# Kernel optimization log

Measured on AMD Instinct MI355X. Metric: run time of the kernel, lower is better.

Reference implementation:

```python
import jax, jax.numpy as jnp
from jax import lax
import numpy as np
import math

B = 8
SEQ_LEN = 2048
LABEL_LEN = 1024
PRED_LEN = 1024
DEC_LEN = LABEL_LEN + PRED_LEN
ENC_IN = 7; DEC_IN = 7; C_OUT = 7
D_MODEL = 512; N_HEADS = 8; D_FF = 512
E_LAYERS = 3; D_LAYERS = 2
MOVING_AVG = 25; FACTOR = 5


def _fixed_table(n, d):
    # sinusoidal FixedEmbedding table (non-learned)
    pos = np.arange(n, dtype=np.float32)[:, None]
    div = np.exp(np.arange(0, d, 2, dtype=np.float32) * (-math.log(10000.0) / d))
    w = np.zeros((n, d), np.float32)
    w[:, 0::2] = np.sin(pos * div)
    w[:, 1::2] = np.cos(pos * div)
    return jnp.asarray(w)

MONTH_T = _fixed_table(13, D_MODEL)
DAY_T = _fixed_table(32, D_MODEL)
WEEKDAY_T = _fixed_table(7, D_MODEL)
HOUR_T = _fixed_table(24, D_MODEL)


def temporal_embed(x_mark):  # [B,L,4] int -> [B,L,D]
    return (MONTH_T[x_mark[..., 0]] + DAY_T[x_mark[..., 1]]
            + WEEKDAY_T[x_mark[..., 2]] + HOUR_T[x_mark[..., 3]])


def circ_conv3(x, W):  # Conv1d(k=3, pad=1, circular, no bias); x [B,L,Cin], W [3,Cin,Cout]
    xp = jnp.concatenate([x[:, -1:], x, x[:, :1]], axis=1)
    return xp[:, :-2] @ W[0] + xp[:, 1:-1] @ W[1] + xp[:, 2:] @ W[2]


def series_decomp(x, k=MOVING_AVG):  # moving-average decomposition
    pad = (k - 1) // 2
    xp = jnp.concatenate([jnp.repeat(x[:, :1], pad, axis=1), x,
                          jnp.repeat(x[:, -1:], pad, axis=1)], axis=1)
    mov = lax.reduce_window(xp, 0.0, lax.add, (1, k, 1), (1, 1, 1), 'VALID') / k
    return x - mov, mov


def my_layernorm(x, w, b):  # LayerNorm then subtract seasonal (time-mean) bias
    mu = jnp.mean(x, axis=-1, keepdims=True)
    var = jnp.var(x, axis=-1, keepdims=True)
    xh = (x - mu) * lax.rsqrt(var + 1e-5) * w + b
    return xh - jnp.mean(xh, axis=1, keepdims=True)


def gelu(x):
    return jax.nn.gelu(x, approximate=False)


def autocorrelation(q, k, v):  # q [B,L,H,E], k/v [B,S,H,E]
    Bq, L, H, E = q.shape
    S = k.shape[1]
    if L > S:
        k = jnp.pad(k, ((0, 0), (0, L - S), (0, 0), (0, 0)))
        v = jnp.pad(v, ((0, 0), (0, L - S), (0, 0), (0, 0)))
    else:
        k = k[:, :L]; v = v[:, :L]
    qf = jnp.fft.rfft(q.transpose(0, 2, 3, 1), axis=-1)  # [B,H,E,Lf]
    kf = jnp.fft.rfft(k.transpose(0, 2, 3, 1), axis=-1)
    corr = jnp.fft.irfft(qf * jnp.conj(kf), n=L, axis=-1)  # [B,H,E,L]
    vv = v.transpose(0, 2, 3, 1)  # [B,H,E,L]
    top_k = int(FACTOR * math.log(L))
    mean_value = jnp.mean(corr, axis=(1, 2))  # [B,L]
    index = lax.top_k(jnp.mean(mean_value, axis=0), top_k)[1]  # [top_k], shared over batch (training path)
    tmp_corr = jax.nn.softmax(mean_value[:, index], axis=-1)  # [B,top_k]
    base = jnp.arange(L)
    def step(acc, iw):
        idx, w = iw
        pattern = jnp.take(vv, (base + idx) % L, axis=-1)  # roll by -idx
        return acc + pattern * w[:, None, None, None], None
    agg, _ = lax.scan(step, jnp.zeros_like(vv), (index, tmp_corr.T))
    return agg.transpose(0, 3, 1, 2)  # [B,L,H,E]


def attn_layer(qx, kx, vx, Wq, bq, Wk, bk, Wv, bv, Wo, bo):
    Bq, L, _ = qx.shape
    S = kx.shape[1]
    q = (qx @ Wq + bq).reshape(Bq, L, N_HEADS, -1)
    k = (kx @ Wk + bk).reshape(Bq, S, N_HEADS, -1)
    v = (vx @ Wv + bv).reshape(Bq, S, N_HEADS, -1)
    out = autocorrelation(q, k, v).reshape(Bq, L, -1)
    return out @ Wo + bo


def _forward(x_enc, x_dec, emb_enc_W, emb_dec_W,
             enc_Wq, enc_bq, enc_Wk, enc_bk, enc_Wv, enc_bv, enc_Wo, enc_bo,
             enc_c1, enc_c2, enc_norm_w, enc_norm_b,
             dec_sWq, dec_sbq, dec_sWk, dec_sbk, dec_sWv, dec_sbv, dec_sWo, dec_sbo,
             dec_cWq, dec_cbq, dec_cWk, dec_cbk, dec_cWv, dec_cbv, dec_cWo, dec_cbo,
             dec_c1, dec_c2, dec_trendW, dec_norm_w, dec_norm_b, proj_W, proj_b,
             x_mark_enc, x_mark_dec):
    Bq = x_enc.shape[0]
    mean = jnp.broadcast_to(jnp.mean(x_enc, axis=1, keepdims=True), (Bq, PRED_LEN, x_enc.shape[2]))
    seasonal_init, trend_init = series_decomp(x_enc)
    trend_init = jnp.concatenate([trend_init[:, -LABEL_LEN:], mean], axis=1)
    zeros = jnp.zeros((Bq, PRED_LEN, x_dec.shape[2]), x_enc.dtype)
    seasonal_init = jnp.concatenate([seasonal_init[:, -LABEL_LEN:], zeros], axis=1)

    # encoder
    enc_out = circ_conv3(x_enc, emb_enc_W) + temporal_embed(x_mark_enc)
    for l in range(E_LAYERS):
        new_x = attn_layer(enc_out, enc_out, enc_out,
                           enc_Wq[l], enc_bq[l], enc_Wk[l], enc_bk[l],
                           enc_Wv[l], enc_bv[l], enc_Wo[l], enc_bo[l])
        x, _ = series_decomp(enc_out + new_x)
        y = gelu(x @ enc_c1[l]) @ enc_c2[l]
        enc_out, _ = series_decomp(x + y)
    enc_out = my_layernorm(enc_out, enc_norm_w, enc_norm_b)

    # decoder
    dec_out = circ_conv3(seasonal_init, emb_dec_W) + temporal_embed(x_mark_dec)
    trend = trend_init
    for l in range(D_LAYERS):
        x = dec_out + attn_layer(dec_out, dec_out, dec_out,
                                 dec_sWq[l], dec_sbq[l], dec_sWk[l], dec_sbk[l],
                                 dec_sWv[l], dec_sbv[l], dec_sWo[l], dec_sbo[l])
        x, t1 = series_decomp(x)
        x = x + attn_layer(x, enc_out, enc_out,
                           dec_cWq[l], dec_cbq[l], dec_cWk[l], dec_cbk[l],
                           dec_cWv[l], dec_cbv[l], dec_cWo[l], dec_cbo[l])
        x, t2 = series_decomp(x)
        y = gelu(x @ dec_c1[l]) @ dec_c2[l]
        dec_out, t3 = series_decomp(x + y)
        trend = trend + circ_conv3(t1 + t2 + t3, dec_trendW[l])  # d_model -> c_out
    dec_out = my_layernorm(dec_out, dec_norm_w, dec_norm_b)
    seasonal_part = dec_out @ proj_W + proj_b
    out = trend + seasonal_part
    return out[:, -PRED_LEN:, :]


def setup_inputs() -> dict:
    key = jax.random.key(0)
    keys = jax.random.split(key, 60)
    ki = iter(range(60))
    def rn(*s):
        return jax.random.normal(keys[next(ki)], s, dtype=jnp.float32) * 0.02
    inp = {}
    inp['x_enc'] = jax.random.normal(keys[next(ki)], (B, SEQ_LEN, ENC_IN), dtype=jnp.float32)
    inp['x_mark_enc'] = jax.random.randint(keys[next(ki)], (B, SEQ_LEN, 4), 0, 7)
    inp['x_dec'] = jax.random.normal(keys[next(ki)], (B, DEC_LEN, DEC_IN), dtype=jnp.float32)
    inp['x_mark_dec'] = jax.random.randint(keys[next(ki)], (B, DEC_LEN, 4), 0, 7)
    inp['emb_enc_W'] = rn(3, ENC_IN, D_MODEL)
    inp['emb_dec_W'] = rn(3, DEC_IN, D_MODEL)
    for n in ('Wq', 'Wk', 'Wv', 'Wo'):
        bn = 'b' + n[1]
        inp['enc_' + n] = rn(E_LAYERS, D_MODEL, D_MODEL)
        inp['enc_' + bn] = rn(E_LAYERS, D_MODEL)
        inp['dec_s' + n] = rn(D_LAYERS, D_MODEL, D_MODEL)
        inp['dec_s' + bn] = rn(D_LAYERS, D_MODEL)
        inp['dec_c' + n] = rn(D_LAYERS, D_MODEL, D_MODEL)
        inp['dec_c' + bn] = rn(D_LAYERS, D_MODEL)
    inp['enc_c1'] = rn(E_LAYERS, D_MODEL, D_FF)
    inp['enc_c2'] = rn(E_LAYERS, D_FF, D_MODEL)
    inp['enc_norm_w'] = jnp.ones((D_MODEL,), jnp.float32)
    inp['enc_norm_b'] = jnp.zeros((D_MODEL,), jnp.float32)
    inp['dec_c1'] = rn(D_LAYERS, D_MODEL, D_FF)
    inp['dec_c2'] = rn(D_LAYERS, D_FF, D_MODEL)
    inp['dec_trendW'] = rn(D_LAYERS, 3, D_MODEL, C_OUT)
    inp['dec_norm_w'] = jnp.ones((D_MODEL,), jnp.float32)
    inp['dec_norm_b'] = jnp.zeros((D_MODEL,), jnp.float32)
    inp['proj_W'] = rn(D_MODEL, C_OUT)
    inp['proj_b'] = jnp.zeros((C_OUT,), jnp.float32)
    return inp


def reference(x_enc, x_mark_enc, x_dec, x_mark_dec, emb_enc_W, emb_dec_W,
              enc_Wq, enc_bq, enc_Wk, enc_bk, enc_Wv, enc_bv, enc_Wo, enc_bo,
              enc_c1, enc_c2, enc_norm_w, enc_norm_b,
              dec_sWq, dec_sbq, dec_sWk, dec_sbk, dec_sWv, dec_sbv, dec_sWo, dec_sbo,
              dec_cWq, dec_cbq, dec_cWk, dec_cbk, dec_cWv, dec_cbv, dec_cWo, dec_cbo,
              dec_c1, dec_c2, dec_trendW, dec_norm_w, dec_norm_b, proj_W, proj_b):
    return _forward(x_enc, x_dec, emb_enc_W, emb_dec_W,
                    enc_Wq, enc_bq, enc_Wk, enc_bk, enc_Wv, enc_bv, enc_Wo, enc_bo,
                    enc_c1, enc_c2, enc_norm_w, enc_norm_b,
                    dec_sWq, dec_sbq, dec_sWk, dec_sbk, dec_sWv, dec_sbv, dec_sWo, dec_sbo,
                    dec_cWq, dec_cbq, dec_cWk, dec_cbk, dec_cWv, dec_cbv, dec_cWo, dec_cbo,
                    dec_c1, dec_c2, dec_trendW, dec_norm_w, dec_norm_b, proj_W, proj_b,
                    x_mark_enc, x_mark_dec)
```

## Files before the change

kernel.cpp:

```cpp
#include <hip/hip_runtime.h>
#include <math.h>

#define BATCH 8
#define LSEQ 2048
#define DMODEL 512
#define TOPK 38
#define MROWS (BATCH * LSEQ)

typedef __attribute__((ext_vector_type(8))) short bf16x8;
typedef __attribute__((ext_vector_type(4))) float f32x4;

__device__ __forceinline__ float wave_sum(float v) {
#pragma unroll
  for (int off = 32; off > 0; off >>= 1) v += __shfl_down(v, off);
  return v;
}

__device__ __forceinline__ short f2bf(float f) {
  unsigned u = __float_as_uint(f);
  unsigned r = (u + 0x7fffu + ((u >> 16) & 1u)) >> 16;
  return (short)r;
}

__global__ void table_init_kernel(float* __restrict__ tab, float2* __restrict__ twg) {
  int i = blockIdx.x * 256 + threadIdx.x;
  if (i < 7 * DMODEL) {
    int p = i >> 9;
    int d = i & (DMODEL - 1);
    float div = expf((float)(d >> 1) * (-2.0f * 9.210340371976184f / 512.0f));
    float ang = (float)p * div;
    tab[i] = (d & 1) ? cosf(ang) : sinf(ang);
  }
  if (i < 1024) {
    float ang = -6.283185307179586f * (float)i / 2048.0f;
    float sn, cs;
    sincosf(ang, &sn, &cs);
    twg[i] = make_float2(cs, sn);
  }
}

__global__ __launch_bounds__(256) void embed_kernel(
    const float* __restrict__ x,
    const float* __restrict__ W,
    const int* __restrict__ mark,
    const float* __restrict__ tab,
    float* __restrict__ out)
{
  __shared__ float xs[21];
  int bt = blockIdx.x;
  int b = bt >> 11, t = bt & (LSEQ - 1);
  int tid = threadIdx.x;
  if (tid < 21) {
    int j = tid / 7, c = tid - j * 7;
    int row = (t - 1 + j + LSEQ) & (LSEQ - 1);
    xs[tid] = x[((size_t)b * LSEQ + row) * 7 + c];
  }
  __syncthreads();
  const int* mk = mark + ((size_t)b * LSEQ + t) * 4;
  int m0 = mk[0], m1 = mk[1], m2 = mk[2], m3 = mk[3];
#pragma unroll
  for (int h = 0; h < 2; ++h) {
    int d = tid + h * 256;
    float acc = tab[m0 * DMODEL + d] + tab[m1 * DMODEL + d] +
                tab[m2 * DMODEL + d] + tab[m3 * DMODEL + d];
#pragma unroll
    for (int j = 0; j < 3; ++j)
#pragma unroll
      for (int c = 0; c < 7; ++c)
        acc += xs[j * 7 + c] * W[(size_t)((j * 7 + c) * DMODEL) + d];
    out[((size_t)b * LSEQ + t) * DMODEL + d] = acc;
  }
}

__global__ void decomp_kernel(const float* __restrict__ x, float* __restrict__ seas,
                              float* __restrict__ trend, int D, int mode)
{
  int bt = blockIdx.x;
  int b = bt >> 11, t = bt & (LSEQ - 1);
  const float* xb = x + (size_t)b * LSEQ * D;
  for (int d = threadIdx.x; d < D; d += blockDim.x) {
    float s = 0.f;
#pragma unroll
    for (int o = -12; o <= 12; ++o) {
      int tt = t + o;
      tt = tt < 0 ? 0 : (tt > LSEQ - 1 ? LSEQ - 1 : tt);
      s += xb[(size_t)tt * D + d];
    }
    float mov = s / 25.0f;
    size_t idx = ((size_t)b * LSEQ + t) * D + d;
    seas[idx] = x[idx] - mov;
    if (mode == 1) trend[idx] = mov;
    else if (mode == 2) trend[idx] += mov;
  }
}

__global__ __launch_bounds__(256) void sgemm_kernel(
    const float* __restrict__ A, const float* __restrict__ B,
    const float* __restrict__ bias, float* __restrict__ C,
    int M, int N, int K)
{
  __shared__ float As[16][132];
  __shared__ float Bs[16][132];
  int m0 = blockIdx.x * 128;
  int n0 = blockIdx.y * 128;
  int tid = threadIdx.x;
  int tx = tid & 15, ty = tid >> 4;
  float acc[8][8];
#pragma unroll
  for (int i = 0; i < 8; ++i)
#pragma unroll
    for (int j = 0; j < 8; ++j) acc[i][j] = 0.f;

  int ar = tid >> 2;
  int ac = (tid & 3) << 2;
  int br = tid >> 5;
  int bc = (tid & 31) << 2;

  for (int k0 = 0; k0 < K; k0 += 16) {
    float4 a0 = *(const float4*)(A + (size_t)(m0 + ar) * K + k0 + ac);
    float4 a1 = *(const float4*)(A + (size_t)(m0 + 64 + ar) * K + k0 + ac);
    float4 b0 = *(const float4*)(B + (size_t)(k0 + br) * N + n0 + bc);
    float4 b1 = *(const float4*)(B + (size_t)(k0 + 8 + br) * N + n0 + bc);
    As[ac + 0][ar] = a0.x; As[ac + 1][ar] = a0.y; As[ac + 2][ar] = a0.z; As[ac + 3][ar] = a0.w;
    As[ac + 0][64 + ar] = a1.x; As[ac + 1][64 + ar] = a1.y; As[ac + 2][64 + ar] = a1.z; As[ac + 3][64 + ar] = a1.w;
    *(float4*)&Bs[br][bc] = b0;
    *(float4*)&Bs[br + 8][bc] = b1;
    __syncthreads();
#pragma unroll
    for (int k = 0; k < 16; ++k) {
      float av[8], bv[8];
      *(float4*)(av)     = *(const float4*)&As[k][ty * 8];
      *(float4*)(av + 4) = *(const float4*)&As[k][ty * 8 + 4];
      *(float4*)(bv)     = *(const float4*)&Bs[k][tx * 8];
      *(float4*)(bv + 4) = *(const float4*)&Bs[k][tx * 8 + 4];
#pragma unroll
      for (int i = 0; i < 8; ++i)
#pragma unroll
        for (int j = 0; j < 8; ++j)
          acc[i][j] = fmaf(av[i], bv[j], acc[i][j]);
    }
    __syncthreads();
  }
#pragma unroll
  for (int i = 0; i < 8; ++i) {
    int m = m0 + ty * 8 + i;
    float* cr = C + (size_t)m * N + n0 + tx * 8;
#pragma unroll
    for (int j = 0; j < 8; j += 4) {
      float4 v = make_float4(acc[i][j], acc[i][j + 1], acc[i][j + 2], acc[i][j + 3]);
      if (bias) {
        const float* bp = bias + n0 + tx * 8 + j;
        v.x += bp[0]; v.y += bp[1]; v.z += bp[2]; v.w += bp[3];
      }
      *(float4*)(cr + j) = v;
    }
  }
}

__global__ void prep_wt_kernel(const float* __restrict__ W, short* __restrict__ Wt) {
  __shared__ float tile[32][33];
  int k0 = blockIdx.x << 5, n0 = blockIdx.y << 5;
  for (int i = threadIdx.y; i < 32; i += 8)
    tile[i][threadIdx.x] = W[(size_t)(k0 + i) * DMODEL + n0 + threadIdx.x];
  __syncthreads();
  for (int i = threadIdx.y; i < 32; i += 8)
    Wt[(size_t)(n0 + i) * DMODEL + k0 + threadIdx.x] = f2bf(tile[threadIdx.x][i]);
}

__global__ __launch_bounds__(256) void gemm_bf16_kernel(
    const float* __restrict__ A, const short* __restrict__ Wt,
    const float* __restrict__ bias, float* __restrict__ C)
{
  const int K = DMODEL, N = DMODEL;
  __shared__ short As[128][40];
  __shared__ short Bs[128][40];
  int m0 = blockIdx.x * 128;
  int n0 = blockIdx.y * 128;
  int tid = threadIdx.x;
  int lane = tid & 63;
  int wave = tid >> 6;
  int wm = (wave >> 1) * 64;
  int wn = (wave & 1) * 64;
  int lr = lane & 15;
  int lk = (lane >> 4) * 8;

  f32x4 acc[4][4];
#pragma unroll
  for (int i = 0; i < 4; ++i)
#pragma unroll
    for (int j = 0; j < 4; ++j) acc[i][j] = (f32x4){0.f, 0.f, 0.f, 0.f};

  for (int k0 = 0; k0 < K; k0 += 32) {
#pragma unroll
    for (int i = 0; i < 4; ++i) {
      int f = tid + i * 256;
      int row = f >> 3, c4 = (f & 7) << 2;
      float4 v = *(const float4*)(A + (size_t)(m0 + row) * K + k0 + c4);
      short4 s = make_short4(f2bf(v.x), f2bf(v.y), f2bf(v.z), f2bf(v.w));
      *(short4*)&As[row][c4] = s;
    }
#pragma unroll
    for (int i = 0; i < 2; ++i) {
      int f = tid + i * 256;
      int row = f >> 2, c8 = (f & 3) << 3;
      *(int4*)&Bs[row][c8] = *(const int4*)(Wt + (size_t)(n0 + row) * K + k0 + c8);
    }
    __syncthreads();
    bf16x8 af[4], bfr[4];
#pragma unroll
    for (int m = 0; m < 4; ++m) af[m] = *(const bf16x8*)&As[wm + m * 16 + lr][lk];
#pragma unroll
    for (int n = 0; n < 4; ++n) bfr[n] = *(const bf16x8*)&Bs[wn + n * 16 + lr][lk];
#pragma unroll
    for (int m = 0; m < 4; ++m)
#pragma unroll
      for (int n = 0; n < 4; ++n)
        acc[m][n] = __builtin_amdgcn_mfma_f32_16x16x32_bf16(af[m], bfr[n], acc[m][n], 0, 0, 0);
    __syncthreads();
  }
  int orow = m0 + wm + (lane >> 4) * 4;
  int ocol = n0 + wn + lr;
#pragma unroll
  for (int m = 0; m < 4; ++m)
#pragma unroll
    for (int n = 0; n < 4; ++n) {
      int col = ocol + n * 16;
      float bv = bias ? bias[col] : 0.f;
#pragma unroll
      for (int r = 0; r < 4; ++r)
        C[(size_t)(orow + m * 16 + r) * N + col] = acc[m][n][r] + bv;
    }
}

__global__ void transpose_kernel(const float* __restrict__ in, float* __restrict__ out) {
  __shared__ float tile[32][33];
  int b = blockIdx.x;
  int r0 = blockIdx.y << 5;
  int c0 = blockIdx.z << 5;
  const float* ib = in + (size_t)b * LSEQ * DMODEL;
  float* ob = out + (size_t)b * LSEQ * DMODEL;
  for (int i = threadIdx.y; i < 32; i += 8)
    tile[i][threadIdx.x] = ib[(size_t)(r0 + i) * DMODEL + c0 + threadIdx.x];
  __syncthreads();
  for (int i = threadIdx.y; i < 32; i += 8)
    ob[(size_t)(c0 + i) * LSEQ + r0 + threadIdx.x] = tile[threadIdx.x][i];
}

__device__ __forceinline__ void fft2048_lds(float2* buf, const float2* tw, int tid, int inverse) {
#pragma unroll 1
  for (int s = 1; s <= 11; ++s) {
    int half = 1 << (s - 1);
#pragma unroll 1
    for (int bf = tid; bf < 1024; bf += 256) {
      int j = bf & (half - 1);
      int i0 = ((bf >> (s - 1)) << s) | j;
      int i1 = i0 + half;
      float2 w = tw[j << (11 - s)];
      float wy = inverse ? -w.y : w.y;
      float2 a = buf[i0], b = buf[i1];
      float tr = b.x * w.x - b.y * wy;
      float ti = b.x * wy + b.y * w.x;
      buf[i0] = make_float2(a.x + tr, a.y + ti);
      buf[i1] = make_float2(a.x - tr, a.y - ti);
    }
    __syncthreads();
  }
}

__global__ __launch_bounds__(256) void corr_spectrum_kernel(
    const float* __restrict__ qt, const float* __restrict__ kt,
    const float2* __restrict__ twg, float2* __restrict__ partial)
{
  __shared__ float2 buf[2048];
  __shared__ float2 acc[2048];
  __shared__ float2 twl[1024];
  int tid = threadIdx.x;
  int b = blockIdx.x >> 6;
  int g = blockIdx.x & 63;
  for (int i = tid; i < 1024; i += 256) twl[i] = twg[i];
  for (int i = tid; i < 2048; i += 256) acc[i] = make_float2(0.f, 0.f);
  __syncthreads();
#pragma unroll 1
  for (int ch = 0; ch < 8; ++ch) {
    int d = (g << 3) + ch;
    const float* qr = qt + ((size_t)b * DMODEL + d) * LSEQ;
    const float* kr = kt + ((size_t)b * DMODEL + d) * LSEQ;
    for (int i = tid; i < 2048; i += 256) {
      int rev = __brev((unsigned)i) >> 21;
      buf[rev] = make_float2(qr[i], kr[i]);
    }
    __syncthreads();
    fft2048_lds(buf, twl, tid, 0);
    for (int i = tid; i < 2048; i += 256) {
      float2 z1 = buf[i];
      float2 z2 = buf[(2048 - i) & 2047];
      float Qr = 0.5f * (z1.x + z2.x);
      float Qi = 0.5f * (z1.y - z2.y);
      float Kr = 0.5f * (z1.y + z2.y);
      float Ki = -0.5f * (z1.x - z2.x);
      acc[i].x += Qr * Kr + Qi * Ki;
      acc[i].y += Qi * Kr - Qr * Ki;
    }
    __syncthreads();
  }
  float2* op = partial + (size_t)blockIdx.x * 2048;
  for (int i = tid; i < 2048; i += 256) op[i] = acc[i];
}

__global__ __launch_bounds__(256) void reduce_partials_kernel(
    const float2* __restrict__ partial, float2* __restrict__ spec)
{
  int b = blockIdx.x;
  int i = blockIdx.y * 256 + threadIdx.x;
  const float2* pp = partial + ((size_t)b * 64) * 2048 + i;
  float sx = 0.f, sy = 0.f;
#pragma unroll 8
  for (int g = 0; g < 64; ++g) {
    float2 v = pp[(size_t)g * 2048];
    sx += v.x; sy += v.y;
  }
  spec[(size_t)b * 2048 + i] = make_float2(sx, sy);
}

__global__ __launch_bounds__(256) void ifft_kernel(
    const float2* __restrict__ spec, const float2* __restrict__ twg,
    float* __restrict__ mv)
{
  __shared__ float2 buf[2048];
  __shared__ float2 twl[1024];
  int tid = threadIdx.x;
  int b = blockIdx.x;
  for (int i = tid; i < 1024; i += 256) twl[i] = twg[i];
  for (int i = tid; i < 2048; i += 256) {
    int rev = __brev((unsigned)i) >> 21;
    buf[rev] = spec[(size_t)b * 2048 + i];
  }
  __syncthreads();
  fft2048_lds(buf, twl, tid, 1);
  const float scale = 1.0f / (2048.0f * 512.0f);
  for (int i = tid; i < 2048; i += 256) mv[(size_t)b * 2048 + i] = buf[i].x * scale;
}

__global__ void topk_kernel(const float* __restrict__ mv, int* __restrict__ idxOut,
                            float* __restrict__ wOut)
{
  __shared__ float cm[2048];
  __shared__ float rmax[256];
  __shared__ int rIdx[256];
  __shared__ int sIdx[TOPK];
  int tid = threadIdx.x;
  for (int i = tid; i < 2048; i += 256) {
    float s = 0.f;
#pragma unroll
    for (int b = 0; b < BATCH; ++b) s += mv[(size_t)b * 2048 + i];
    cm[i] = s;
  }
  __syncthreads();
  for (int it = 0; it < TOPK; ++it) {
    float best = -1e30f; int bi = 0;
    for (int i = tid; i < 2048; i += 256)
      if (cm[i] > best) { best = cm[i]; bi = i; }
    rmax[tid] = best; rIdx[tid] = bi;
    __syncthreads();
    for (int s = 128; s > 0; s >>= 1) {
      if (tid < s && rmax[tid + s] > rmax[tid]) { rmax[tid] = rmax[tid + s]; rIdx[tid] = rIdx[tid + s]; }
      __syncthreads();
    }
    if (tid == 0) { sIdx[it] = rIdx[0]; idxOut[it] = rIdx[0]; cm[rIdx[0]] = -1e30f; }
    __syncthreads();
  }
  if (tid < BATCH) {
    int b = tid;
    float vals[TOPK];
    float m = -1e30f;
    for (int j = 0; j < TOPK; ++j) { vals[j] = mv[(size_t)b * 2048 + sIdx[j]]; m = fmaxf(m, vals[j]); }
    float s = 0.f;
    for (int j = 0; j < TOPK; ++j) { vals[j] = expf(vals[j] - m); s += vals[j]; }
    for (int j = 0; j < TOPK; ++j) wOut[b * TOPK + j] = vals[j] / s;
  }
}

__global__ __launch_bounds__(256) void shift_sum_kernel(
    const float* __restrict__ v, const int* __restrict__ idx,
    const float* __restrict__ w, float* __restrict__ out)
{
  __shared__ int sidx[TOPK];
  __shared__ float sw[TOPK];
  int bt = blockIdx.x;
  int b = bt & 7, t = bt >> 3;
  int tid = threadIdx.x;
  if (tid < TOPK) { sidx[tid] = idx[tid]; sw[tid] = w[b * TOPK + tid]; }
  __syncthreads();
  float a0 = 0.f, a1 = 0.f;
  const float* vb = v + (size_t)b * LSEQ * DMODEL;
#pragma unroll 1
  for (int j = 0; j < TOPK; ++j) {
    int row = (t + sidx[j]) & (LSEQ - 1);
    const float* vr = vb + (size_t)row * DMODEL;
    a0 = fmaf(sw[j], vr[tid], a0);
    a1 = fmaf(sw[j], vr[tid + 256], a1);
  }
  size_t o = ((size_t)b * LSEQ + t) * DMODEL;
  out[o + tid] = a0;
  out[o + tid + 256] = a1;
}

__global__ void add_kernel(const float* __restrict__ a, const float* __restrict__ b,
                           float* __restrict__ c, int n4)
{
  int i = blockIdx.x * blockDim.x + threadIdx.x;
  int stride = gridDim.x * blockDim.x;
  const float4* A = (const float4*)a;
  const float4* B = (const float4*)b;
  float4* C = (float4*)c;
  for (; i < n4; i += stride) {
    float4 x = A[i], y = B[i];
    C[i] = make_float4(x.x + y.x, x.y + y.y, x.z + y.z, x.w + y.w);
  }
}

__global__ void gelu_kernel(float* __restrict__ x, int n4) {
  int i = blockIdx.x * blockDim.x + threadIdx.x;
  int stride = gridDim.x * blockDim.x;
  float4* X = (float4*)x;
  const float k = 0.7071067811865475f;
  for (; i < n4; i += stride) {
    float4 v = X[i];
    v.x = 0.5f * v.x * (1.f + erff(v.x * k));
    v.y = 0.5f * v.y * (1.f + erff(v.y * k));
    v.z = 0.5f * v.z * (1.f + erff(v.z * k));
    v.w = 0.5f * v.w * (1.f + erff(v.w * k));
    X[i] = v;
  }
}

__global__ __launch_bounds__(256) void layernorm_kernel(
    const float* __restrict__ x, const float* __restrict__ w,
    const float* __restrict__ bb, float* __restrict__ out)
{
  __shared__ float red[256];
  int row = blockIdx.x;
  int tid = threadIdx.x;
  const float* xr = x + (size_t)row * DMODEL;
  float v0 = xr[tid], v1 = xr[tid + 256];
  red[tid] = v0 + v1;
  __syncthreads();
  for (int o = 128; o > 0; o >>= 1) {
    if (tid < o) red[tid] += red[tid + o];
    __syncthreads();
  }
  float mu = red[0] / 512.0f;
  __syncthreads();
  float d0 = v0 - mu, d1 = v1 - mu;
  red[tid] = d0 * d0 + d1 * d1;
  __syncthreads();
  for (int o = 128; o > 0; o >>= 1) {
    if (tid < o) red[tid] += red[tid + o];
    __syncthreads();
  }
  float var = red[0] / 512.0f;
  float inv = 1.0f / sqrtf(var + 1e-5f);
  out[(size_t)row * DMODEL + tid] = d0 * inv * w[tid] + bb[tid];
  out[(size_t)row * DMODEL + tid + 256] = d1 * inv * w[tid + 256] + bb[tid + 256];
}

__global__ __launch_bounds__(256) void colsum_kernel(const float* __restrict__ x,
                                                     float* __restrict__ part)
{
  int b = blockIdx.x, ch = blockIdx.y;
  const float* xb = x + ((size_t)b * LSEQ + (size_t)ch * 128) * DMODEL;
  float s0 = 0.f, s1 = 0.f;
#pragma unroll 1
  for (int t = 0; t < 128; ++t) {
    s0 += xb[(size_t)t * DMODEL + threadIdx.x];
    s1 += xb[(size_t)t * DMODEL + threadIdx.x + 256];
  }
  part[(size_t)(b * 16 + ch) * DMODEL + threadIdx.x] = s0;
  part[(size_t)(b * 16 + ch) * DMODEL + threadIdx.x + 256] = s1;
}

__global__ void colmean_finish_kernel(const float* __restrict__ part, float* __restrict__ mu) {
  int i = blockIdx.x * 256 + threadIdx.x;
  if (i < BATCH * DMODEL) {
    int b = i / DMODEL, d = i - b * DMODEL;
    float s = 0.f;
#pragma unroll
    for (int c = 0; c < 16; ++c) s += part[(size_t)(b * 16 + c) * DMODEL + d];
    mu[i] = s / (float)LSEQ;
  }
}

__global__ __launch_bounds__(256) void sub_colmean_kernel(
    const float* __restrict__ x, const float* __restrict__ mu, float* __restrict__ out)
{
  int bt = blockIdx.x;
  int b = bt >> 11;
  size_t base = (size_t)bt * DMODEL;
  int d0 = threadIdx.x, d1 = threadIdx.x + 256;
  out[base + d0] = x[base + d0] - mu[b * DMODEL + d0];
  out[base + d1] = x[base + d1] - mu[b * DMODEL + d1];
}

__global__ void mean_enc_kernel(const float* __restrict__ x, float* __restrict__ mean7) {
  int b = blockIdx.x / 7, c = blockIdx.x % 7;
  float s = 0.f;
  for (int t = threadIdx.x; t < LSEQ; t += 64) s += x[((size_t)b * LSEQ + t) * 7 + c];
  s = wave_sum(s);
  if (threadIdx.x == 0) mean7[b * 7 + c] = s / 2048.0f;
}

__global__ void build_inits_kernel(const float* __restrict__ seas7, const float* __restrict__ trend7,
                                   const float* __restrict__ mean7,
                                   float* __restrict__ seasonal_init, float* __restrict__ trend_acc)
{
  int i = blockIdx.x * 256 + threadIdx.x;
  if (i >= BATCH * LSEQ * 7) return;
  int c = i % 7;
  int bt = i / 7;
  int t = bt & (LSEQ - 1);
  int b = bt >> 11;
  if (t < 1024) {
    size_t src = ((size_t)b * LSEQ + (t + 1024)) * 7 + c;
    seasonal_init[i] = seas7[src];
    trend_acc[i] = trend7[src];
  } else {
    seasonal_init[i] = 0.f;
    trend_acc[i] = mean7[b * 7 + c];
  }
}

__global__ void trend_conv_kernel(const float* __restrict__ x, const float* __restrict__ W,
                                  float* __restrict__ trend)
{
  int bt = blockIdx.x;
  int b = bt >> 11, t = bt & (LSEQ - 1);
  int lane = threadIdx.x;
  float acc[7] = {0, 0, 0, 0, 0, 0, 0};
#pragma unroll
  for (int j = 0; j < 3; ++j) {
    int row = (t - 1 + j + LSEQ) & (LSEQ - 1);
    const float* xr = x + ((size_t)b * LSEQ + row) * DMODEL;
    const float* wj = W + (size_t)j * DMODEL * 7;
    for (int d = lane; d < DMODEL; d += 64) {
      float xv = xr[d];
      const float* wr = wj + d * 7;
#pragma unroll
      for (int c = 0; c < 7; ++c) acc[c] += xv * wr[c];
    }
  }
#pragma unroll
  for (int c = 0; c < 7; ++c) {
    float s = wave_sum(acc[c]);
    if (lane == 0) trend[((size_t)b * LSEQ + t) * 7 + c] += s;
  }
}

__global__ void final_proj_kernel(const float* __restrict__ x, const float* __restrict__ W,
                                  const float* __restrict__ bias, const float* __restrict__ trend,
                                  float* __restrict__ out)
{
  int bt = blockIdx.x;
  int b = bt >> 10, tt = bt & 1023;
  int t = tt + 1024;
  int lane = threadIdx.x;
  const float* xr = x + ((size_t)b * LSEQ + t) * DMODEL;
  float acc[7] = {0, 0, 0, 0, 0, 0, 0};
  for (int d = lane; d < DMODEL; d += 64) {
    float xv = xr[d];
    const float* wr = W + d * 7;
#pragma unroll
    for (int c = 0; c < 7; ++c) acc[c] += xv * wr[c];
  }
#pragma unroll
  for (int c = 0; c < 7; ++c) {
    float s = wave_sum(acc[c]);
    if (lane == 0)
      out[((size_t)b * 1024 + tt) * 7 + c] = s + bias[c] + trend[((size_t)b * LSEQ + t) * 7 + c];
  }
}

static inline void launch_sgemm(const float* A, const float* W, const float* bias, float* C,
                                hipStream_t s)
{
  sgemm_kernel<<<dim3(MROWS / 128, DMODEL / 128), dim3(256), 0, s>>>(
      A, W, bias, C, MROWS, DMODEL, DMODEL);
}

static inline void launch_gemm_bf16(const float* A, const float* W, const float* bias, float* C,
                                    short* wtScratch, hipStream_t s)
{
  prep_wt_kernel<<<dim3(16, 16), dim3(32, 8), 0, s>>>(W, wtScratch);
  gemm_bf16_kernel<<<dim3(MROWS / 128, DMODEL / 128), dim3(256), 0, s>>>(A, wtScratch, bias, C);
}

struct AttnScratch {
  float2* partial;
  float2* spec;
  float* mv;
  int* idx;
  float* w;
  const float2* twg;
  short* wt;
};

static void run_attn(const float* qx, const float* kx, const float* vx,
                     const float* Wq, const float* bq, const float* Wk, const float* bk,
                     const float* Wv, const float* bv, const float* Wo, const float* bo,
                     float* t1, float* t2, float* t3, const AttnScratch& sc, hipStream_t s)
{
  dim3 tg(BATCH, LSEQ / 32, DMODEL / 32);
  launch_sgemm(qx, Wq, bq, t1, s);
  transpose_kernel<<<tg, dim3(32, 8), 0, s>>>(t1, t2);
  launch_sgemm(kx, Wk, bk, t1, s);
  transpose_kernel<<<tg, dim3(32, 8), 0, s>>>(t1, t3);
  launch_gemm_bf16(vx, Wv, bv, t1, sc.wt, s);
  corr_spectrum_kernel<<<dim3(BATCH * 64), dim3(256), 0, s>>>(t2, t3, sc.twg, sc.partial);
  reduce_partials_kernel<<<dim3(BATCH, 8), dim3(256), 0, s>>>(sc.partial, sc.spec);
  ifft_kernel<<<dim3(BATCH), dim3(256), 0, s>>>(sc.spec, sc.twg, sc.mv);
  topk_kernel<<<dim3(1), dim3(256), 0, s>>>(sc.mv, sc.idx, sc.w);
  shift_sum_kernel<<<dim3(MROWS), dim3(256), 0, s>>>(t1, sc.idx, sc.w, t2);
  launch_gemm_bf16(t2, Wo, bo, t3, sc.wt, s);
}

extern "C" void kernel_launch(void* const* d_in, const int* in_sizes, int n_in,
                              void* d_out, int out_size, void* d_ws, size_t ws_size,
                              hipStream_t stream)
{
  if (n_in < 41) return;

  const float* x_enc    = (const float*)d_in[0];
  const int*   mark_enc = (const int*)d_in[1];
  const int*   mark_dec = (const int*)d_in[3];
  const float* emb_enc_W = (const float*)d_in[4];
  const float* emb_dec_W = (const float*)d_in[5];
  const float* enc_Wq = (const float*)d_in[6];
  const float* enc_bq = (const float*)d_in[7];
  const float* dec_sWq = (const float*)d_in[8];
  const float* dec_sbq = (const float*)d_in[9];
  const float* dec_cWq = (const float*)d_in[10];
  const float* dec_cbq = (const float*)d_in[11];
  const float* enc_Wk = (const float*)d_in[12];
  const float* enc_bk = (const float*)d_in[13];
  const float* dec_sWk = (const float*)d_in[14];
  const float* dec_sbk = (const float*)d_in[15];
  const float* dec_cWk = (const float*)d_in[16];
  const float* dec_cbk = (const float*)d_in[17];
  const float* enc_Wv = (const float*)d_in[18];
  const float* enc_bv = (const float*)d_in[19];
  const float* dec_sWv = (const float*)d_in[20];
  const float* dec_sbv = (const float*)d_in[21];
  const float* dec_cWv = (const float*)d_in[22];
  const float* dec_cbv = (const float*)d_in[23];
  const float* enc_Wo = (const float*)d_in[24];
  const float* enc_bo = (const float*)d_in[25];
  const float* dec_sWo = (const float*)d_in[26];
  const float* dec_sbo = (const float*)d_in[27];
  const float* dec_cWo = (const float*)d_in[28];
  const float* dec_cbo = (const float*)d_in[29];
  const float* enc_c1 = (const float*)d_in[30];
  const float* enc_c2 = (const float*)d_in[31];
  const float* enc_nw = (const float*)d_in[32];
  const float* enc_nb = (const float*)d_in[33];
  const float* dec_c1 = (const float*)d_in[34];
  const float* dec_c2 = (const float*)d_in[35];
  const float* dec_trendW = (const float*)d_in[36];
  const float* dec_nw = (const float*)d_in[37];
  const float* dec_nb = (const float*)d_in[38];
  const float* proj_W = (const float*)d_in[39];
  const float* proj_b = (const float*)d_in[40];

  (void)in_sizes; (void)out_size;

  const size_t BIG = (size_t)MROWS * DMODEL * sizeof(float);
  char* p = (char*)d_ws;
  float* enc_out = (float*)p; p += BIG;
  float* dec_out = (float*)p; p += BIG;
  float* tsum    = (float*)p; p += BIG;
  float* b1 = (float*)p; p += BIG;
  float* b2 = (float*)p; p += BIG;
  float* b3 = (float*)p; p += BIG;
  float2* partial = (float2*)p; p += (size_t)BATCH * 64 * 2048 * sizeof(float2);
  float2* specbuf = (float2*)p; p += (size_t)BATCH * 2048 * sizeof(float2);
  short* wtScratch = (short*)p; p += (size_t)DMODEL * DMODEL * sizeof(short);
  float* mv = (float*)p; p += (size_t)BATCH * 2048 * sizeof(float);
  float* tab = (float*)p; p += 7 * DMODEL * sizeof(float);
  float2* twg = (float2*)p; p += 1024 * sizeof(float2);
  float* seas7 = (float*)p; p += (size_t)BATCH * LSEQ * 7 * sizeof(float);
  float* trend7tmp = (float*)p; p += (size_t)BATCH * LSEQ * 7 * sizeof(float);
  float* seasonal_init = (float*)p; p += (size_t)BATCH * LSEQ * 7 * sizeof(float);
  float* trend_acc = (float*)p; p += (size_t)BATCH * LSEQ * 7 * sizeof(float);
  float* colpart = (float*)p; p += (size_t)BATCH * 16 * DMODEL * sizeof(float);
  float* colmu = (float*)p; p += (size_t)BATCH * DMODEL * sizeof(float);
  float* mean7 = (float*)p; p += 256;
  int* idxbuf = (int*)p; p += 256;
  float* wbuf = (float*)p; p += 2048;
  if ((size_t)(p - (char*)d_ws) > ws_size) return;

  const int n4 = MROWS * DMODEL / 4;
  AttnScratch sc{partial, specbuf, mv, idxbuf, wbuf, twg, wtScratch};

  table_init_kernel<<<dim3(14), dim3(256), 0, stream>>>(tab, twg);
  decomp_kernel<<<dim3(MROWS), dim3(64), 0, stream>>>(x_enc, seas7, trend7tmp, 7, 1);
  mean_enc_kernel<<<dim3(56), dim3(64), 0, stream>>>(x_enc, mean7);
  build_inits_kernel<<<dim3((BATCH * LSEQ * 7 + 255) / 256), dim3(256), 0, stream>>>(
      seas7, trend7tmp, mean7, seasonal_init, trend_acc);
  embed_kernel<<<dim3(MROWS), dim3(256), 0, stream>>>(x_enc, emb_enc_W, mark_enc, tab, enc_out);
  embed_kernel<<<dim3(MROWS), dim3(256), 0, stream>>>(seasonal_init, emb_dec_W, mark_dec, tab, dec_out);

  for (int l = 0; l < 3; ++l) {
    size_t wOff = (size_t)l * DMODEL * DMODEL, bOff = (size_t)l * DMODEL;
    run_attn(enc_out, enc_out, enc_out,
             enc_Wq + wOff, enc_bq + bOff, enc_Wk + wOff, enc_bk + bOff,
             enc_Wv + wOff, enc_bv + bOff, enc_Wo + wOff, enc_bo + bOff,
             b1, b2, b3, sc, stream);
    add_kernel<<<dim3(2048), dim3(256), 0, stream>>>(enc_out, b3, b1, n4);
    decomp_kernel<<<dim3(MROWS), dim3(256), 0, stream>>>(b1, b2, nullptr, DMODEL, 0);
    launch_gemm_bf16(b2, enc_c1 + wOff, nullptr, b3, wtScratch, stream);
    gelu_kernel<<<dim3(2048), dim3(256), 0, stream>>>(b3, n4);
    launch_gemm_bf16(b3, enc_c2 + wOff, nullptr, b1, wtScratch, stream);
    add_kernel<<<dim3(2048), dim3(256), 0, stream>>>(b2, b1, b3, n4);
    decomp_kernel<<<dim3(MROWS), dim3(256), 0, stream>>>(b3, enc_out, nullptr, DMODEL, 0);
  }
  layernorm_kernel<<<dim3(MROWS), dim3(256), 0, stream>>>(enc_out, enc_nw, enc_nb, b1);
  colsum_kernel<<<dim3(BATCH, 16), dim3(256), 0, stream>>>(b1, colpart);
  colmean_finish_kernel<<<dim3(16), dim3(256), 0, stream>>>(colpart, colmu);
  sub_colmean_kernel<<<dim3(MROWS), dim3(256), 0, stream>>>(b1, colmu, enc_out);

  for (int l = 0; l < 2; ++l) {
    size_t wOff = (size_t)l * DMODEL * DMODEL, bOff = (size_t)l * DMODEL;
    run_attn(dec_out, dec_out, dec_out,
             dec_sWq + wOff, dec_sbq + bOff, dec_sWk + wOff, dec_sbk + bOff,
             dec_sWv + wOff, dec_sbv + bOff, dec_sWo + wOff, dec_sbo + bOff,
             b1, b2, b3, sc, stream);
    add_kernel<<<dim3(2048), dim3(256), 0, stream>>>(dec_out, b3, b1, n4);
    decomp_kernel<<<dim3(MROWS), dim3(256), 0, stream>>>(b1, b2, tsum, DMODEL, 1);
    run_attn(b2, enc_out, enc_out,
             dec_cWq + wOff, dec_cbq + bOff, dec_cWk + wOff, dec_cbk + bOff,
             dec_cWv + wOff, dec_cbv + bOff, dec_cWo + wOff, dec_cbo + bOff,
             b1, b3, dec_out, sc, stream);
    add_kernel<<<dim3(2048), dim3(256), 0, stream>>>(b2, dec_out, b1, n4);
    decomp_kernel<<<dim3(MROWS), dim3(256), 0, stream>>>(b1, b3, tsum, DMODEL, 2);
    launch_gemm_bf16(b3, dec_c1 + wOff, nullptr, b1, wtScratch, stream);
    gelu_kernel<<<dim3(2048), dim3(256), 0, stream>>>(b1, n4);
    launch_gemm_bf16(b1, dec_c2 + wOff, nullptr, b2, wtScratch, stream);
    add_kernel<<<dim3(2048), dim3(256), 0, stream>>>(b3, b2, b1, n4);
    decomp_kernel<<<dim3(MROWS), dim3(256), 0, stream>>>(b1, dec_out, tsum, DMODEL, 2);
    trend_conv_kernel<<<dim3(MROWS), dim3(64), 0, stream>>>(
        tsum, dec_trendW + (size_t)l * 3 * DMODEL * 7, trend_acc);
  }
  layernorm_kernel<<<dim3(MROWS), dim3(256), 0, stream>>>(dec_out, dec_nw, dec_nb, b1);
  colsum_kernel<<<dim3(BATCH, 16), dim3(256), 0, stream>>>(b1, colpart);
  colmean_finish_kernel<<<dim3(16), dim3(256), 0, stream>>>(colpart, colmu);
  sub_colmean_kernel<<<dim3(MROWS), dim3(256), 0, stream>>>(b1, colmu, b2);
  final_proj_kernel<<<dim3(BATCH * 1024), dim3(64), 0, stream>>>(
      b2, proj_W, proj_b, trend_acc, (float*)d_out);
}
```

Before: 5.080 ms.

## Batch bf16 weight prep, tile moving-average decomp in LDS, halve sgemm M-tile

Converts every bf16-path weight matrix to transposed bf16 once at startup instead of before each GEMM. Replaces the 512-wide decomposition kernel with a tiled version that stages a 56-row window in shared memory, so the 25-tap moving average reads global memory once per element. Halves the fp32 sgemm row tile to 64 to launch more blocks. The costs are extra workspace for all converted weights and more per-block B-tile reloads in the sgemm.

```diff
diff --git a/kernel.cpp b/kernel.cpp
--- a/kernel.cpp
+++ b/kernel.cpp
@@ -6,6 +6,7 @@
 #define DMODEL 512
 #define TOPK 38
 #define MROWS (BATCH * LSEQ)
+#define WSLOT (DMODEL * DMODEL)
 
 typedef __attribute__((ext_vector_type(8))) short bf16x8;
 typedef __attribute__((ext_vector_type(4))) float f32x4;
@@ -72,23 +73,54 @@
   }
 }
 
-__global__ void decomp_kernel(const float* __restrict__ x, float* __restrict__ seas,
-                              float* __restrict__ trend, int D, int mode)
+__global__ void decomp7_kernel(const float* __restrict__ x, float* __restrict__ seas,
+                               float* __restrict__ trend)
 {
   int bt = blockIdx.x;
   int b = bt >> 11, t = bt & (LSEQ - 1);
-  const float* xb = x + (size_t)b * LSEQ * D;
-  for (int d = threadIdx.x; d < D; d += blockDim.x) {
+  const float* xb = x + (size_t)b * LSEQ * 7;
+  for (int d = threadIdx.x; d < 7; d += blockDim.x) {
     float s = 0.f;
 #pragma unroll
     for (int o = -12; o <= 12; ++o) {
       int tt = t + o;
       tt = tt < 0 ? 0 : (tt > LSEQ - 1 ? LSEQ - 1 : tt);
-      s += xb[(size_t)tt * D + d];
+      s += xb[(size_t)tt * 7 + d];
     }
     float mov = s / 25.0f;
-    size_t idx = ((size_t)b * LSEQ + t) * D + d;
+    size_t idx = ((size_t)b * LSEQ + t) * 7 + d;
     seas[idx] = x[idx] - mov;
+    trend[idx] = mov;
+  }
+}
+
+__global__ __launch_bounds__(256) void decomp512_kernel(
+    const float* __restrict__ x, float* __restrict__ seas,
+    float* __restrict__ trend, int mode)
+{
+  __shared__ float ls[56][256];
+  int tc = blockIdx.x;
+  int b = blockIdx.y;
+  int dh = blockIdx.z;
+  int tid = threadIdx.x;
+  int d = dh * 256 + tid;
+  const float* xb = x + (size_t)b * LSEQ * DMODEL;
+  int t0 = tc * 32;
+#pragma unroll 1
+  for (int r = 0; r < 56; ++r) {
+    int tg = t0 - 12 + r;
+    tg = tg < 0 ? 0 : (tg > LSEQ - 1 ? LSEQ - 1 : tg);
+    ls[r][tid] = xb[(size_t)tg * DMODEL + d];
+  }
+  __syncthreads();
+#pragma unroll 1
+  for (int tl = 0; tl < 32; ++tl) {
+    float s = 0.f;
+#pragma unroll
+    for (int o = -12; o <= 12; ++o) s += ls[tl + 12 + o][tid];
+    float mov = s / 25.0f;
+    size_t idx = ((size_t)b * LSEQ + t0 + tl) * DMODEL + d;
+    seas[idx] = ls[tl + 12][tid] - mov;
     if (mode == 1) trend[idx] = mov;
     else if (mode == 2) trend[idx] += mov;
   }
@@ -99,15 +131,15 @@
     const float* __restrict__ bias, float* __restrict__ C,
     int M, int N, int K)
 {
-  __shared__ float As[16][132];
+  __shared__ float As[16][68];
   __shared__ float Bs[16][132];
-  int m0 = blockIdx.x * 128;
+  int m0 = blockIdx.x * 64;
   int n0 = blockIdx.y * 128;
   int tid = threadIdx.x;
   int tx = tid & 15, ty = tid >> 4;
-  float acc[8][8];
-#pragma unroll
-  for (int i = 0; i < 8; ++i)
+  float acc[4][8];
+#pragma unroll
+  for (int i = 0; i < 4; ++i)
 #pragma unroll
     for (int j = 0; j < 8; ++j) acc[i][j] = 0.f;
 
@@ -118,23 +150,20 @@
 
   for (int k0 = 0; k0 < K; k0 += 16) {
     float4 a0 = *(const float4*)(A + (size_t)(m0 + ar) * K + k0 + ac);
-    float4 a1 = *(const float4*)(A + (size_t)(m0 + 64 + ar) * K + k0 + ac);
     float4 b0 = *(const float4*)(B + (size_t)(k0 + br) * N + n0 + bc);
     float4 b1 = *(const float4*)(B + (size_t)(k0 + 8 + br) * N + n0 + bc);
     As[ac + 0][ar] = a0.x; As[ac + 1][ar] = a0.y; As[ac + 2][ar] = a0.z; As[ac + 3][ar] = a0.w;
-    As[ac + 0][64 + ar] = a1.x; As[ac + 1][64 + ar] = a1.y; As[ac + 2][64 + ar] = a1.z; As[ac + 3][64 + ar] = a1.w;
     *(float4*)&Bs[br][bc] = b0;
     *(float4*)&Bs[br + 8][bc] = b1;
     __syncthreads();
 #pragma unroll
     for (int k = 0; k < 16; ++k) {
-      float av[8], bv[8];
-      *(float4*)(av)     = *(const float4*)&As[k][ty * 8];
-      *(float4*)(av + 4) = *(const float4*)&As[k][ty * 8 + 4];
+      float av[4], bv[8];
+      *(float4*)(av)     = *(const float4*)&As[k][ty * 4];
       *(float4*)(bv)     = *(const float4*)&Bs[k][tx * 8];
       *(float4*)(bv + 4) = *(const float4*)&Bs[k][tx * 8 + 4];
 #pragma unroll
-      for (int i = 0; i < 8; ++i)
+      for (int i = 0; i < 4; ++i)
 #pragma unroll
         for (int j = 0; j < 8; ++j)
           acc[i][j] = fmaf(av[i], bv[j], acc[i][j]);
@@ -142,8 +171,8 @@
     __syncthreads();
   }
 #pragma unroll
-  for (int i = 0; i < 8; ++i) {
-    int m = m0 + ty * 8 + i;
+  for (int i = 0; i < 4; ++i) {
+    int m = m0 + ty * 4 + i;
     float* cr = C + (size_t)m * N + n0 + tx * 8;
 #pragma unroll
     for (int j = 0; j < 8; j += 4) {
@@ -157,14 +186,17 @@
   }
 }
 
-__global__ void prep_wt_kernel(const float* __restrict__ W, short* __restrict__ Wt) {
+__global__ void prep_wt_multi_kernel(const float* __restrict__ W, short* __restrict__ Wt) {
   __shared__ float tile[32][33];
+  int layer = blockIdx.z;
+  const float* src = W + (size_t)layer * WSLOT;
+  short* dst = Wt + (size_t)layer * WSLOT;
   int k0 = blockIdx.x << 5, n0 = blockIdx.y << 5;
   for (int i = threadIdx.y; i < 32; i += 8)
-    tile[i][threadIdx.x] = W[(size_t)(k0 + i) * DMODEL + n0 + threadIdx.x];
+    tile[i][threadIdx.x] = src[(size_t)(k0 + i) * DMODEL + n0 + threadIdx.x];
   __syncthreads();
   for (int i = threadIdx.y; i < 32; i += 8)
-    Wt[(size_t)(n0 + i) * DMODEL + k0 + threadIdx.x] = f2bf(tile[threadIdx.x][i]);
+    dst[(size_t)(n0 + i) * DMODEL + k0 + threadIdx.x] = f2bf(tile[threadIdx.x][i]);
 }
 
 __global__ __launch_bounds__(256) void gemm_bf16_kernel(
@@ -582,15 +614,20 @@
 static inline void launch_sgemm(const float* A, const float* W, const float* bias, float* C,
                                 hipStream_t s)
 {
-  sgemm_kernel<<<dim3(MROWS / 128, DMODEL / 128), dim3(256), 0, s>>>(
+  sgemm_kernel<<<dim3(MROWS / 64, DMODEL / 128), dim3(256), 0, s>>>(
       A, W, bias, C, MROWS, DMODEL, DMODEL);
 }
 
-static inline void launch_gemm_bf16(const float* A, const float* W, const float* bias, float* C,
-                                    short* wtScratch, hipStream_t s)
-{
-  prep_wt_kernel<<<dim3(16, 16), dim3(32, 8), 0, s>>>(W, wtScratch);
-  gemm_bf16_kernel<<<dim3(MROWS / 128, DMODEL / 128), dim3(256), 0, s>>>(A, wtScratch, bias, C);
+static inline void launch_gemm_bf16(const float* A, const short* Wt, const float* bias, float* C,
+                                    hipStream_t s)
+{
+  gemm_bf16_kernel<<<dim3(MROWS / 128, DMODEL / 128), dim3(256), 0, s>>>(A, Wt, bias, C);
+}
+
+static inline void launch_decomp512(const float* x, float* seas, float* trend, int mode,
+                                    hipStream_t s)
+{
+  decomp512_kernel<<<dim3(64, BATCH, 2), dim3(256), 0, s>>>(x, seas, trend, mode);
 }
 
 struct AttnScratch {
@@ -600,12 +637,11 @@
   int* idx;
   float* w;
   const float2* twg;
-  short* wt;
 };
 
 static void run_attn(const float* qx, const float* kx, const float* vx,
                      const float* Wq, const float* bq, const float* Wk, const float* bk,
-                     const float* Wv, const float* bv, const float* Wo, const float* bo,
+                     const short* wtV, const float* bv, const short* wtO, const float* bo,
                      float* t1, float* t2, float* t3, const AttnScratch& sc, hipStream_t s)
 {
   dim3 tg(BATCH, LSEQ / 32, DMODEL / 32);
@@ -613,13 +649,13 @@
   transpose_kernel<<<tg, dim3(32, 8), 0, s>>>(t1, t2);
   launch_sgemm(kx, Wk, bk, t1, s);
   transpose_kernel<<<tg, dim3(32, 8), 0, s>>>(t1, t3);
-  launch_gemm_bf16(vx, Wv, bv, t1, sc.wt, s);
+  launch_gemm_bf16(vx, wtV, bv, t1, s);
   corr_spectrum_kernel<<<dim3(BATCH * 64), dim3(256), 0, s>>>(t2, t3, sc.twg, sc.partial);
   reduce_partials_kernel<<<dim3(BATCH, 8), dim3(256), 0, s>>>(sc.partial, sc.spec);
   ifft_kernel<<<dim3(BATCH), dim3(256), 0, s>>>(sc.spec, sc.twg, sc.mv);
   topk_kernel<<<dim3(1), dim3(256), 0, s>>>(sc.mv, sc.idx, sc.w);
   shift_sum_kernel<<<dim3(MROWS), dim3(256), 0, s>>>(t1, sc.idx, sc.w, t2);
-  launch_gemm_bf16(t2, Wo, bo, t3, sc.wt, s);
+  launch_gemm_bf16(t2, wtO, bo, t3, s);
 }
 
 extern "C" void kernel_launch(void* const* d_in, const int* in_sizes, int n_in,
@@ -681,7 +717,7 @@
   float* b3 = (float*)p; p += BIG;
   float2* partial = (float2*)p; p += (size_t)BATCH * 64 * 2048 * sizeof(float2);
   float2* specbuf = (float2*)p; p += (size_t)BATCH * 2048 * sizeof(float2);
-  short* wtScratch = (short*)p; p += (size_t)DMODEL * DMODEL * sizeof(short);
+  short* wtAll = (short*)p; p += (size_t)24 * WSLOT * sizeof(short);
   float* mv = (float*)p; p += (size_t)BATCH * 2048 * sizeof(float);
   float* tab = (float*)p; p += 7 * DMODEL * sizeof(float);
   float2* twg = (float2*)p; p += 1024 * sizeof(float2);
@@ -697,10 +733,31 @@
   if ((size_t)(p - (char*)d_ws) > ws_size) return;
 
   const int n4 = MROWS * DMODEL / 4;
-  AttnScratch sc{partial, specbuf, mv, idxbuf, wbuf, twg, wtScratch};
+  AttnScratch sc{partial, specbuf, mv, idxbuf, wbuf, twg};
+
+  short* wt_enc_Wv = wtAll + (size_t)0 * WSLOT;
+  short* wt_enc_Wo = wtAll + (size_t)3 * WSLOT;
+  short* wt_enc_c1 = wtAll + (size_t)6 * WSLOT;
+  short* wt_enc_c2 = wtAll + (size_t)9 * WSLOT;
+  short* wt_dec_sWv = wtAll + (size_t)12 * WSLOT;
+  short* wt_dec_sWo = wtAll + (size_t)14 * WSLOT;
+  short* wt_dec_cWv = wtAll + (size_t)16 * WSLOT;
+  short* wt_dec_cWo = wtAll + (size_t)18 * WSLOT;
+  short* wt_dec_c1 = wtAll + (size_t)20 * WSLOT;
+  short* wt_dec_c2 = wtAll + (size_t)22 * WSLOT;
 
   table_init_kernel<<<dim3(14), dim3(256), 0, stream>>>(tab, twg);
-  decomp_kernel<<<dim3(MROWS), dim3(64), 0, stream>>>(x_enc, seas7, trend7tmp, 7, 1);
+  prep_wt_multi_kernel<<<dim3(16, 16, 3), dim3(32, 8), 0, stream>>>(enc_Wv, wt_enc_Wv);
+  prep_wt_multi_kernel<<<dim3(16, 16, 3), dim3(32, 8), 0, stream>>>(enc_Wo, wt_enc_Wo);
+  prep_wt_multi_kernel<<<dim3(16, 16, 3), dim3(32, 8), 0, stream>>>(enc_c1, wt_enc_c1);
+  prep_wt_multi_kernel<<<dim3(16, 16, 3), dim3(32, 8), 0, stream>>>(enc_c2, wt_enc_c2);
+  prep_wt_multi_kernel<<<dim3(16, 16, 2), dim3(32, 8), 0, stream>>>(dec_sWv, wt_dec_sWv);
+  prep_wt_multi_kernel<<<dim3(16, 16, 2), dim3(32, 8), 0, stream>>>(dec_sWo, wt_dec_sWo);
+  prep_wt_multi_kernel<<<dim3(16, 16, 2), dim3(32, 8), 0, stream>>>(dec_cWv, wt_dec_cWv);
+  prep_wt_multi_kernel<<<dim3(16, 16, 2), dim3(32, 8), 0, stream>>>(dec_cWo, wt_dec_cWo);
+  prep_wt_multi_kernel<<<dim3(16, 16, 2), dim3(32, 8), 0, stream>>>(dec_c1, wt_dec_c1);
+  prep_wt_multi_kernel<<<dim3(16, 16, 2), dim3(32, 8), 0, stream>>>(dec_c2, wt_dec_c2);
+  decomp7_kernel<<<dim3(MROWS), dim3(64), 0, stream>>>(x_enc, seas7, trend7tmp);
   mean_enc_kernel<<<dim3(56), dim3(64), 0, stream>>>(x_enc, mean7);
   build_inits_kernel<<<dim3((BATCH * LSEQ * 7 + 255) / 256), dim3(256), 0, stream>>>(
       seas7, trend7tmp, mean7, seasonal_init, trend_acc);
@@ -708,18 +765,18 @@
   embed_kernel<<<dim3(MROWS), dim3(256), 0, stream>>>(seasonal_init, emb_dec_W, mark_dec, tab, dec_out);
 
   for (int l = 0; l < 3; ++l) {
-    size_t wOff = (size_t)l * DMODEL * DMODEL, bOff = (size_t)l * DMODEL;
+    size_t wOff = (size_t)l * WSLOT, bOff = (size_t)l * DMODEL;
     run_attn(enc_out, enc_out, enc_out,
              enc_Wq + wOff, enc_bq + bOff, enc_Wk + wOff, enc_bk + bOff,
-             enc_Wv + wOff, enc_bv + bOff, enc_Wo + wOff, enc_bo + bOff,
+             wt_enc_Wv + wOff, enc_bv + bOff, wt_enc_Wo + wOff, enc_bo + bOff,
              b1, b2, b3, sc, stream);
     add_kernel<<<dim3(2048), dim3(256), 0, stream>>>(enc_out, b3, b1, n4);
-    decomp_kernel<<<dim3(MROWS), dim3(256), 0, stream>>>(b1, b2, nullptr, DMODEL, 0);
-    launch_gemm_bf16(b2, enc_c1 + wOff, nullptr, b3, wtScratch, stream);
+    launch_decomp512(b1, b2, nullptr, 0, stream);
+    launch_gemm_bf16(b2, wt_enc_c1 + wOff, nullptr, b3, stream);
     gelu_kernel<<<dim3(2048), dim3(256), 0, stream>>>(b3, n4);
-    launch_gemm_bf16(b3, enc_c2 + wOff, nullptr, b1, wtScratch, stream);
+    launch_gemm_bf16(b3, wt_enc_c2 + wOff, nullptr, b1, stream);
     add_kernel<<<dim3(2048), dim3(256), 0, stream>>>(b2, b1, b3, n4);
-    decomp_kernel<<<dim3(MROWS), dim3(256), 0, stream>>>(b3, enc_out, nullptr, DMODEL, 0);
+    launch_decomp512(b3, enc_out, nullptr, 0, stream);
   }
   layernorm_kernel<<<dim3(MROWS), dim3(256), 0, stream>>>(enc_out, enc_nw, enc_nb, b1);
   colsum_kernel<<<dim3(BATCH, 16), dim3(256), 0, stream>>>(b1, colpart);
@@ -727,24 +784,24 @@
   sub_colmean_kernel<<<dim3(MROWS), dim3(256), 0, stream>>>(b1, colmu, enc_out);
 
   for (int l = 0; l < 2; ++l) {
-    size_t wOff = (size_t)l * DMODEL * DMODEL, bOff = (size_t)l * DMODEL;
+    size_t wOff = (size_t)l * WSLOT, bOff = (size_t)l * DMODEL;
     run_attn(dec_out, dec_out, dec_out,
              dec_sWq + wOff, dec_sbq + bOff, dec_sWk + wOff, dec_sbk + bOff,
-             dec_sWv + wOff, dec_sbv + bOff, dec_sWo + wOff, dec_sbo + bOff,
+             wt_dec_sWv + wOff, dec_sbv + bOff, wt_dec_sWo + wOff, dec_sbo + bOff,
              b1, b2, b3, sc, stream);
     add_kernel<<<dim3(2048), dim3(256), 0, stream>>>(dec_out, b3, b1, n4);
-    decomp_kernel<<<dim3(MROWS), dim3(256), 0, stream>>>(b1, b2, tsum, DMODEL, 1);
+    launch_decomp512(b1, b2, tsum, 1, stream);
     run_attn(b2, enc_out, enc_out,
              dec_cWq + wOff, dec_cbq + bOff, dec_cWk + wOff, dec_cbk + bOff,
-             dec_cWv + wOff, dec_cbv + bOff, dec_cWo + wOff, dec_cbo + bOff,
+             wt_dec_cWv + wOff, dec_cbv + bOff, wt_dec_cWo + wOff, dec_cbo + bOff,
              b1, b3, dec_out, sc, stream);
     add_kernel<<<dim3(2048), dim3(256), 0, stream>>>(b2, dec_out, b1, n4);
-    decomp_kernel<<<dim3(MROWS), dim3(256), 0, stream>>>(b1, b3, tsum, DMODEL, 2);
-    launch_gemm_bf16(b3, dec_c1 + wOff, nullptr, b1, wtScratch, stream);
+    launch_decomp512(b1, b3, tsum, 2, stream);
+    launch_gemm_bf16(b3, wt_dec_c1 + wOff, nullptr, b1, stream);
     gelu_kernel<<<dim3(2048), dim3(256), 0, stream>>>(b1, n4);
-    launch_gemm_bf16(b1, dec_c2 + wOff, nullptr, b2, wtScratch, stream);
+    launch_gemm_bf16(b1, wt_dec_c2 + wOff, nullptr, b2, stream);
     add_kernel<<<dim3(2048), dim3(256), 0, stream>>>(b3, b2, b1, n4);
-    decomp_kernel<<<dim3(MROWS), dim3(256), 0, stream>>>(b1, dec_out, tsum, DMODEL, 2);
+    launch_decomp512(b1, dec_out, tsum, 2, stream);
     trend_conv_kernel<<<dim3(MROWS), dim3(64), 0, stream>>>(
         tsum, dec_trendW + (size_t)l * 3 * DMODEL * 7, trend_acc);
   }
```

After: 5.126 ms. No clear change (+0.9%).
